# Kernel optimization log

Measured on AMD Instinct MI355X. Metric: run time of the kernel, lower is better.

## Reference

```python
import jax, jax.numpy as jnp
import numpy as np
from jax import lax

N_NODES = 19
N_FILT = 8
CONV_CH = N_NODES * N_FILT  # 152
T = 512
POOL = 4
T_POOL = T // POOL  # 128
GCN_OUT = 16
FLAT = N_NODES * GCN_OUT * T_POOL  # 38912
HID = 128
N_CLS = 2
BN_EPS = 1e-5


def setup_inputs() -> dict:
    key = jax.random.key(0)
    ks = jax.random.split(key, 12)
    B = 1024
    x = jax.random.normal(ks[0], (B, N_NODES, T), dtype=jnp.float32)
    # grouped Conv1d(19 -> 152, k=5, groups=19): kernel (out_ch, in_ch/groups=1, k)
    conv_w = jax.random.normal(ks[1], (CONV_CH, 1, 5), dtype=jnp.float32) * 0.2
    conv_b = jax.random.normal(ks[2], (CONV_CH,), dtype=jnp.float32) * 0.05
    bn_gamma = jnp.ones((CONV_CH,), jnp.float32)
    bn_beta = jnp.zeros((CONV_CH,), jnp.float32)
    bn_mean = jax.random.normal(ks[3], (CONV_CH,), dtype=jnp.float32) * 0.1
    bn_var = jax.random.uniform(ks[4], (CONV_CH,), dtype=jnp.float32, minval=0.5, maxval=1.5)
    adj = jax.random.uniform(ks[5], (N_NODES, N_NODES), dtype=jnp.float32)
    gcn_w = jax.random.normal(ks[6], (GCN_OUT, N_FILT), dtype=jnp.float32) * (1.0 / np.sqrt(N_FILT))
    gcn_b = jnp.zeros((GCN_OUT,), jnp.float32)
    w1 = jax.random.normal(ks[7], (HID, FLAT), dtype=jnp.float32) * (1.0 / np.sqrt(FLAT))
    b1 = jnp.zeros((HID,), jnp.float32)
    w2 = jax.random.normal(ks[8], (N_CLS, HID), dtype=jnp.float32) * (1.0 / np.sqrt(HID))
    b2 = jnp.zeros((N_CLS,), jnp.float32)
    return dict(x=x, conv_w=conv_w, conv_b=conv_b, bn_gamma=bn_gamma, bn_beta=bn_beta,
                bn_mean=bn_mean, bn_var=bn_var, adj=adj, gcn_w=gcn_w, gcn_b=gcn_b,
                w1=w1, b1=b1, w2=w2, b2=b2)


def reference(x, conv_w, conv_b, bn_gamma, bn_beta, bn_mean, bn_var, adj,
              gcn_w, gcn_b, w1, b1, w2, b2):
    B = x.shape[0]
    # depthwise temporal conv: [B,19,T] -> [B,152,T]
    h = lax.conv_general_dilated(x, conv_w, window_strides=(1,), padding=[(2, 2)],
                                 feature_group_count=N_NODES,
                                 dimension_numbers=('NCW', 'OIW', 'NCW'))
    h = h + conv_b[None, :, None]
    # BatchNorm1d (eval mode: running stats) + ReLU, fused elementwise
    inv = bn_gamma / jnp.sqrt(bn_var + BN_EPS)
    h = jax.nn.relu(h * inv[None, :, None] + (bn_beta - bn_mean * inv)[None, :, None])
    # MaxPool1d(4): [B,152,512] -> [B,152,128]
    h = h.reshape(B, CONV_CH, T_POOL, POOL).max(axis=-1)
    # view -> [B,19,8,128]
    h = h.reshape(B, N_NODES, N_FILT, T_POOL)
    # softmax adjacency aggregation: bift = A_ij * bjft
    A = jax.nn.softmax(adj, axis=1)
    support = jnp.einsum('ij,bjft->bift', A, h)
    # permute to [B,19,128,8], linear 8->16, ReLU
    g = jax.nn.relu(jnp.einsum('bnft,of->bnto', support, gcn_w) + gcn_b)
    # classifier: flatten -> Linear(38912,128) -> ReLU -> (Dropout eval=identity) -> Linear(128,2)
    flat = g.reshape(B, FLAT)
    hid = jax.nn.relu(flat @ w1.T + b1)
    return hid @ w2.T + b2
```

## Files before the change

### kernel.cpp

```cpp
#include <hip/hip_runtime.h>

#define NB    1024
#define NN    19
#define NF    8
#define CCH   152
#define TLEN  512
#define TP    128
#define GO    16
#define KFLAT 38912
#define HID   128
#define NCLS  2
#define NROWS (NB*TP)
#define KC    152
#define KP    160
#define NJP   20
#define NOUT  304
#define GW    320
#define KW    (TP*GW)

#define KTILE 1024
#define NKT   (KW / KTILE)

typedef float  f32x4  __attribute__((ext_vector_type(4)));
typedef __bf16 bf16x8 __attribute__((ext_vector_type(8)));
typedef __bf16 bf16x4 __attribute__((ext_vector_type(4)));
typedef unsigned short u16x8 __attribute__((ext_vector_type(8)));

__global__ __launch_bounds__(256) void prep_small(
    const float* __restrict__ adj,
    const float* __restrict__ bn_gamma, const float* __restrict__ bn_beta,
    const float* __restrict__ bn_mean,  const float* __restrict__ bn_var,
    const float* __restrict__ conv_b,
    float* __restrict__ A_g, float* __restrict__ bnS, float* __restrict__ bnB)
{
    const int tid = threadIdx.x;
    if (tid < NN) {
        float v[NN];
        float m = -1e30f;
        #pragma unroll
        for (int j = 0; j < NN; ++j) { v[j] = adj[tid * NN + j]; m = fmaxf(m, v[j]); }
        float s = 0.f;
        #pragma unroll
        for (int j = 0; j < NN; ++j) { v[j] = expf(v[j] - m); s += v[j]; }
        float rc = 1.f / s;
        #pragma unroll
        for (int j = 0; j < NN; ++j) A_g[tid * NN + j] = v[j] * rc;
    }
    if (tid >= 64 && tid < 64 + CCH) {
        int c = tid - 64;
        float inv = bn_gamma[c] * rsqrtf(bn_var[c] + 1e-5f);
        bnS[c] = inv;
        bnB[c] = conv_b[c] * inv + bn_beta[c] - bn_mean[c] * inv;
    }
}

__global__ __launch_bounds__(256) void prep_m2(
    const float* __restrict__ A_g, const float* __restrict__ gcn_w,
    __bf16* __restrict__ m2g)
{
    int i = blockIdx.x * 256 + threadIdx.x;
    if (i >= GW * KP) return;
    int c = i / KP, k = i - c * KP;
    float v = 0.f;
    if (c < NOUT && k < KC) {
        int n = c >> 4, o = c & 15;
        int j = k >> 3, f = k & 7;
        v = A_g[n * NN + j] * gcn_w[o * NF + f];
    }
    m2g[i] = (__bf16)v;
}

__global__ __launch_bounds__(640) void conv_mix(
    const float* __restrict__ x,
    const float* __restrict__ conv_w,
    const float* __restrict__ bnS, const float* __restrict__ bnB,
    const __bf16* __restrict__ m2g,
    const float* __restrict__ gcn_b,
    __bf16* __restrict__ g2)
{
    __shared__ __align__(16) __bf16 Hs[NJP][64][8];

    const int tid  = threadIdx.x;
    const int lane = tid & 63, w = tid >> 6;
    const int b    = blockIdx.x >> 1;
    const int half = blockIdx.x & 1;
    const int tp0  = half * 64;

    {
        const int T = tp0 + lane;
        #pragma unroll
        for (int k = 0; k < 2; ++k) {
            const int n = 2 * w + k;
            if (n < NN) {
                const float* xr = x + ((size_t)b * NN + n) * TLEN;
                float4 L0 = {0.f, 0.f, 0.f, 0.f};
                float4 L2 = {0.f, 0.f, 0.f, 0.f};
                if (T > 0)   L0 = *(const float4*)(xr + 4 * T - 4);
                float4 L1 =       *(const float4*)(xr + 4 * T);
                if (T < 127) L2 = *(const float4*)(xr + 4 * T + 4);
                float xv[9] = {L0.z, L0.w, L1.x, L1.y, L1.z, L1.w, L2.x, L2.y, L2.z};

                const float* cw = conv_w + n * (NF * 5);
                const float* Sp = bnS + n * NF;
                const float* Bp = bnB + n * NF;
                union { __bf16 h[8]; u16x8 v; } hv;
                #pragma unroll
                for (int f = 0; f < NF; ++f) {
                    float w0 = cw[f*5+0], w1 = cw[f*5+1], w2 = cw[f*5+2], w3 = cw[f*5+3], w4 = cw[f*5+4];
                    float s = Sp[f], bb = Bp[f];
                    float m = -1e30f;
                    #pragma unroll
                    for (int p = 0; p < 4; ++p) {
                        float a = xv[p]*w0 + xv[p+1]*w1 + xv[p+2]*w2 + xv[p+3]*w3 + xv[p+4]*w4;
                        m = fmaxf(m, a * s + bb);
                    }
                    hv.h[f] = (__bf16)fmaxf(m, 0.f);
                }
                *(u16x8*)&Hs[n][lane][0] = hv.v;
            } else {
                u16x8 z = {0,0,0,0,0,0,0,0};
                *(u16x8*)&Hs[NJP - 1][lane][0] = z;
            }
        }
    }

    const int arow = lane & 15;
    const int jg   = lane >> 4;
    const int ct0  = w * 2;
    const float4 gbv = *(const float4*)(gcn_b + jg * 4);

    bf16x8 mf[2][5];
    #pragma unroll
    for (int ct = 0; ct < 2; ++ct)
        #pragma unroll
        for (int ks = 0; ks < 5; ++ks)
            mf[ct][ks] = *(const bf16x8*)(
                m2g + (size_t)((ct0 + ct) * 16 + arow) * KP + ks * 32 + jg * 8);

    __syncthreads();

    for (int it = 0; it < 4; ++it) {
        const int tl = it * 16 + arow;

        bf16x8 af[5];
        #pragma unroll
        for (int ks = 0; ks < 5; ++ks)
            af[ks] = *(const bf16x8*)&Hs[ks * 4 + jg][tl][0];

        f32x4 acc[2];
        #pragma unroll
        for (int ct = 0; ct < 2; ++ct) acc[ct] = (f32x4){0.f, 0.f, 0.f, 0.f};

        #pragma unroll
        for (int ks = 0; ks < 5; ++ks)
            #pragma unroll
            for (int ct = 0; ct < 2; ++ct)
                acc[ct] = __builtin_amdgcn_mfma_f32_16x16x32_bf16(mf[ct][ks], af[ks], acc[ct], 0, 0, 0);

        __bf16* gp = g2 + ((size_t)b * TP + tp0 + tl) * GW + ct0 * 16 + jg * 4;
        #pragma unroll
        for (int ct = 0; ct < 2; ++ct) {
            bf16x4 v;
            v[0] = (__bf16)fmaxf(acc[ct][0] + gbv.x, 0.f);
            v[1] = (__bf16)fmaxf(acc[ct][1] + gbv.y, 0.f);
            v[2] = (__bf16)fmaxf(acc[ct][2] + gbv.z, 0.f);
            v[3] = (__bf16)fmaxf(acc[ct][3] + gbv.w, 0.f);
            *(bf16x4*)(gp + ct * 16) = v;
        }
    }
}

__global__ __launch_bounds__(256) void w1_permute(
    const float* __restrict__ w1, __bf16* __restrict__ w1p)
{
    int i = blockIdx.x * 256 + threadIdx.x;
    if (i >= HID * (KW / 8)) return;
    int j = i / 5120, rem = i - j * 5120;
    int t = rem / 40, c8 = rem - t * 40;
    bf16x8 r;
    if (c8 < 38) {
        int n = c8 >> 1, o0 = (c8 & 1) * 8;
        const float* src = w1 + (size_t)j * KFLAT + n * 2048 + t * 16 + o0;
        #pragma unroll
        for (int e = 0; e < 8; ++e) r[e] = (__bf16)src[e];
    } else {
        #pragma unroll
        for (int e = 0; e < 8; ++e) r[e] = (__bf16)0.f;
    }
    *(bf16x8*)(w1p + (size_t)i * 8) = r;
}

__global__ __launch_bounds__(256) void gemm_fc1(
    const __bf16* __restrict__ gmat,
    const __bf16* __restrict__ wmat,
    float* __restrict__ partial)
{
    __shared__ __align__(16) __bf16 At[128][40];
    __shared__ __align__(16) __bf16 Bt[128][40];

    const int tid = threadIdx.x;
    const int b0 = blockIdx.x * 128;
    const int k0 = blockIdx.y * KTILE;

    const int lane = tid & 63;
    const int w = tid >> 6;
    const int wm = (w >> 1) * 64;
    const int wn = (w & 1) * 64;

    const int srow = tid >> 2;
    const int soct = tid & 3;

    f32x4 acc[4][4];
    #pragma unroll
    for (int m = 0; m < 4; ++m)
        #pragma unroll
        for (int n = 0; n < 4; ++n) acc[m][n] = (f32x4){0.f, 0.f, 0.f, 0.f};

    const int arow = lane & 15;
    const int aoct = (lane >> 4) * 8;

    for (int ks = 0; ks < KTILE / 32; ++ks) {
        const int gk = k0 + ks * 32 + soct * 8;
        *(u16x8*)&At[srow     ][soct * 8] = *(const u16x8*)(gmat + (size_t)(b0 + srow     ) * KW + gk);
        *(u16x8*)&At[srow + 64][soct * 8] = *(const u16x8*)(gmat + (size_t)(b0 + srow + 64) * KW + gk);
        *(u16x8*)&Bt[srow     ][soct * 8] = *(const u16x8*)(wmat + (size_t)(srow     ) * KW + gk);
        *(u16x8*)&Bt[srow + 64][soct * 8] = *(const u16x8*)(wmat + (size_t)(srow + 64) * KW + gk);
        __syncthreads();

        bf16x8 af[4], bfr[4];
        #pragma unroll
        for (int m = 0; m < 4; ++m) af[m]  = *(const bf16x8*)&At[wm + m * 16 + arow][aoct];
        #pragma unroll
        for (int n = 0; n < 4; ++n) bfr[n] = *(const bf16x8*)&Bt[wn + n * 16 + arow][aoct];
        #pragma unroll
        for (int m = 0; m < 4; ++m)
            #pragma unroll
            for (int n = 0; n < 4; ++n)
                acc[m][n] = __builtin_amdgcn_mfma_f32_16x16x32_bf16(af[m], bfr[n], acc[m][n], 0, 0, 0);
        __syncthreads();
    }

    float* pout = partial + (size_t)blockIdx.y * (NB * HID);
    #pragma unroll
    for (int m = 0; m < 4; ++m) {
        const int rbase = b0 + wm + m * 16 + (lane >> 4) * 4;
        #pragma unroll
        for (int n = 0; n < 4; ++n) {
            const int col = wn + n * 16 + (lane & 15);
            #pragma unroll
            for (int r = 0; r < 4; ++r)
                pout[(size_t)(rbase + r) * HID + col] = acc[m][n][r];
        }
    }
}

__global__ __launch_bounds__(128) void reduce_fc2(
    const float* __restrict__ partial,
    const float* __restrict__ b1,
    const float* __restrict__ w2,
    const float* __restrict__ b2,
    float* __restrict__ out)
{
    __shared__ float red0[128], red1[128];
    const int b = blockIdx.x, j = threadIdx.x;
    float s = b1[j];
    #pragma unroll 4
    for (int p = 0; p < NKT; ++p) s += partial[(size_t)p * (NB * HID) + b * HID + j];
    float h = fmaxf(s, 0.f);
    red0[j] = h * w2[j];
    red1[j] = h * w2[HID + j];
    __syncthreads();
    for (int off = 64; off > 0; off >>= 1) {
        if (j < off) { red0[j] += red0[j + off]; red1[j] += red1[j + off]; }
        __syncthreads();
    }
    if (j == 0) {
        out[b * 2 + 0] = red0[0] + b2[0];
        out[b * 2 + 1] = red1[0] + b2[1];
    }
}

extern "C" void kernel_launch(void* const* d_in, const int* in_sizes, int n_in,
                              void* d_out, int out_size, void* d_ws, size_t ws_size,
                              hipStream_t stream) {
    const float* x        = (const float*)d_in[0];
    const float* conv_w   = (const float*)d_in[1];
    const float* conv_b   = (const float*)d_in[2];
    const float* bn_gamma = (const float*)d_in[3];
    const float* bn_beta  = (const float*)d_in[4];
    const float* bn_mean  = (const float*)d_in[5];
    const float* bn_var   = (const float*)d_in[6];
    const float* adj      = (const float*)d_in[7];
    const float* gcn_w    = (const float*)d_in[8];
    const float* gcn_b    = (const float*)d_in[9];
    const float* w1       = (const float*)d_in[10];
    const float* b1       = (const float*)d_in[11];
    const float* w2       = (const float*)d_in[12];
    const float* b2       = (const float*)d_in[13];
    float* out = (float*)d_out;

    char* ws = (char*)d_ws;
    __bf16* g2   = (__bf16*)ws;
    __bf16* w1p  = (__bf16*)(ws + 83886080);
    float*  part = (float*)(ws + 94371840);
    __bf16* m2g  = (__bf16*)(ws + 125829120);
    float*  A_g  = (float*)(ws + 125931520);
    float*  bnS  = (float*)(ws + 125933568);
    float*  bnB  = (float*)(ws + 125934592);

    prep_small<<<dim3(1), dim3(256), 0, stream>>>(
        adj, bn_gamma, bn_beta, bn_mean, bn_var, conv_b, A_g, bnS, bnB);
    prep_m2<<<dim3(200), dim3(256), 0, stream>>>(A_g, gcn_w, m2g);
    conv_mix<<<dim3(NB * 2), dim3(640), 0, stream>>>(x, conv_w, bnS, bnB, m2g, gcn_b, g2);
    w1_permute<<<dim3(HID * (KW / 8) / 256), dim3(256), 0, stream>>>(w1, w1p);
    gemm_fc1<<<dim3(8, NKT), dim3(256), 0, stream>>>(g2, w1p, part);
    reduce_fc2<<<dim3(NB), dim3(128), 0, stream>>>(part, b1, w2, b2, out);
}
```

Before: 117.4 us.

## Make conv_mix persistent over four tiles with double-buffered LDS and prefetch

Each conv_mix block now handles four (batch, half) tiles instead of one, with a double-buffered LDS H tile. The x loads for the next tile are issued before the MFMA mix of the current tile, and the next conv is computed into the other buffer. This amortizes the per-block m2g fragment loads and launch overhead and overlaps global loads with MFMA work. In exchange the grid shrinks by four and register pressure rises from the prefetched float4s.

```diff
diff --git a/kernel.cpp b/kernel.cpp
--- a/kernel.cpp
+++ b/kernel.cpp
@@ -17,6 +17,7 @@
 #define NOUT  304
 #define GW    320
 #define KW    (TP*GW)
+#define NTPB  4
 
 #define KTILE 1024
 #define NKT   (KW / KTILE)
@@ -78,56 +79,17 @@
     const float* __restrict__ gcn_b,
     __bf16* __restrict__ g2)
 {
-    __shared__ __align__(16) __bf16 Hs[NJP][64][8];
+    __shared__ __align__(16) __bf16 Hs[2][NJP][64][8];
 
     const int tid  = threadIdx.x;
     const int lane = tid & 63, w = tid >> 6;
-    const int b    = blockIdx.x >> 1;
-    const int half = blockIdx.x & 1;
-    const int tp0  = half * 64;
-
-    {
-        const int T = tp0 + lane;
-        #pragma unroll
-        for (int k = 0; k < 2; ++k) {
-            const int n = 2 * w + k;
-            if (n < NN) {
-                const float* xr = x + ((size_t)b * NN + n) * TLEN;
-                float4 L0 = {0.f, 0.f, 0.f, 0.f};
-                float4 L2 = {0.f, 0.f, 0.f, 0.f};
-                if (T > 0)   L0 = *(const float4*)(xr + 4 * T - 4);
-                float4 L1 =       *(const float4*)(xr + 4 * T);
-                if (T < 127) L2 = *(const float4*)(xr + 4 * T + 4);
-                float xv[9] = {L0.z, L0.w, L1.x, L1.y, L1.z, L1.w, L2.x, L2.y, L2.z};
-
-                const float* cw = conv_w + n * (NF * 5);
-                const float* Sp = bnS + n * NF;
-                const float* Bp = bnB + n * NF;
-                union { __bf16 h[8]; u16x8 v; } hv;
-                #pragma unroll
-                for (int f = 0; f < NF; ++f) {
-                    float w0 = cw[f*5+0], w1 = cw[f*5+1], w2 = cw[f*5+2], w3 = cw[f*5+3], w4 = cw[f*5+4];
-                    float s = Sp[f], bb = Bp[f];
-                    float m = -1e30f;
-                    #pragma unroll
-                    for (int p = 0; p < 4; ++p) {
-                        float a = xv[p]*w0 + xv[p+1]*w1 + xv[p+2]*w2 + xv[p+3]*w3 + xv[p+4]*w4;
-                        m = fmaxf(m, a * s + bb);
-                    }
-                    hv.h[f] = (__bf16)fmaxf(m, 0.f);
-                }
-                *(u16x8*)&Hs[n][lane][0] = hv.v;
-            } else {
-                u16x8 z = {0,0,0,0,0,0,0,0};
-                *(u16x8*)&Hs[NJP - 1][lane][0] = z;
-            }
-        }
-    }
-
     const int arow = lane & 15;
     const int jg   = lane >> 4;
     const int ct0  = w * 2;
     const float4 gbv = *(const float4*)(gcn_b + jg * 4);
+    const int n0 = 2 * w, n1 = 2 * w + 1;
+
+    const int t0 = blockIdx.x * NTPB;
 
     bf16x8 mf[2][5];
     #pragma unroll
@@ -137,35 +99,94 @@
             mf[ct][ks] = *(const bf16x8*)(
                 m2g + (size_t)((ct0 + ct) * 16 + arow) * KP + ks * 32 + jg * 8);
 
+    float4 nx[3];
+    const float4 f4z = {0.f, 0.f, 0.f, 0.f};
+
+    auto LOADX = [&](int tau) {
+        const int b = tau >> 1;
+        const int T = (tau & 1) * 64 + lane;
+        const float* xr = x + ((size_t)b * NN + n0) * TLEN;
+        nx[0] = (T > 0)   ? *(const float4*)(xr + 4 * T - 4) : f4z;
+        nx[1] =             *(const float4*)(xr + 4 * T);
+        nx[2] = (T < 127) ? *(const float4*)(xr + 4 * T + 4) : f4z;
+    };
+
+    auto CONV1 = [&](int buf, int n, const float4& L0, const float4& L1, const float4& L2) {
+        float xv[9] = {L0.z, L0.w, L1.x, L1.y, L1.z, L1.w, L2.x, L2.y, L2.z};
+        const float* cw = conv_w + n * (NF * 5);
+        const float* Sp = bnS + n * NF;
+        const float* Bp = bnB + n * NF;
+        union { __bf16 h[8]; u16x8 v; } hv;
+        #pragma unroll
+        for (int f = 0; f < NF; ++f) {
+            float w0 = cw[f*5+0], w1 = cw[f*5+1], w2 = cw[f*5+2], w3 = cw[f*5+3], w4 = cw[f*5+4];
+            float s = Sp[f], bb = Bp[f];
+            float m = -1e30f;
+            #pragma unroll
+            for (int p = 0; p < 4; ++p) {
+                float a = xv[p]*w0 + xv[p+1]*w1 + xv[p+2]*w2 + xv[p+3]*w3 + xv[p+4]*w4;
+                m = fmaxf(m, a * s + bb);
+            }
+            hv.h[f] = (__bf16)fmaxf(m, 0.f);
+        }
+        *(u16x8*)&Hs[buf][n][lane][0] = hv.v;
+    };
+
+    auto CONV = [&](int buf, int tau) {
+        const int b = tau >> 1;
+        const int T = (tau & 1) * 64 + lane;
+        CONV1(buf, n0, nx[0], nx[1], nx[2]);
+        if (n1 < NN) {
+            const float* xr = x + ((size_t)b * NN + n1) * TLEN;
+            float4 L0 = (T > 0)   ? *(const float4*)(xr + 4 * T - 4) : f4z;
+            float4 L1 =             *(const float4*)(xr + 4 * T);
+            float4 L2 = (T < 127) ? *(const float4*)(xr + 4 * T + 4) : f4z;
+            CONV1(buf, n1, L0, L1, L2);
+        } else {
+            u16x8 z = {0,0,0,0,0,0,0,0};
+            *(u16x8*)&Hs[buf][NJP - 1][lane][0] = z;
+        }
+    };
+
+    auto MIX = [&](int buf, int tau) {
+        const int b = tau >> 1, tp0 = (tau & 1) * 64;
+        for (int it = 0; it < 4; ++it) {
+            const int tl = it * 16 + arow;
+            bf16x8 af[5];
+            #pragma unroll
+            for (int ks = 0; ks < 5; ++ks)
+                af[ks] = *(const bf16x8*)&Hs[buf][ks * 4 + jg][tl][0];
+            f32x4 acc[2];
+            #pragma unroll
+            for (int ct = 0; ct < 2; ++ct) acc[ct] = (f32x4){0.f, 0.f, 0.f, 0.f};
+            #pragma unroll
+            for (int ks = 0; ks < 5; ++ks)
+                #pragma unroll
+                for (int ct = 0; ct < 2; ++ct)
+                    acc[ct] = __builtin_amdgcn_mfma_f32_16x16x32_bf16(mf[ct][ks], af[ks], acc[ct], 0, 0, 0);
+            __bf16* gp = g2 + ((size_t)b * TP + tp0 + tl) * GW + ct0 * 16 + jg * 4;
+            #pragma unroll
+            for (int ct = 0; ct < 2; ++ct) {
+                bf16x4 v;
+                v[0] = (__bf16)fmaxf(acc[ct][0] + gbv.x, 0.f);
+                v[1] = (__bf16)fmaxf(acc[ct][1] + gbv.y, 0.f);
+                v[2] = (__bf16)fmaxf(acc[ct][2] + gbv.z, 0.f);
+                v[3] = (__bf16)fmaxf(acc[ct][3] + gbv.w, 0.f);
+                *(bf16x4*)(gp + ct * 16) = v;
+            }
+        }
+    };
+
+    LOADX(t0);
+    CONV(0, t0);
     __syncthreads();
 
-    for (int it = 0; it < 4; ++it) {
-        const int tl = it * 16 + arow;
-
-        bf16x8 af[5];
-        #pragma unroll
-        for (int ks = 0; ks < 5; ++ks)
-            af[ks] = *(const bf16x8*)&Hs[ks * 4 + jg][tl][0];
-
-        f32x4 acc[2];
-        #pragma unroll
-        for (int ct = 0; ct < 2; ++ct) acc[ct] = (f32x4){0.f, 0.f, 0.f, 0.f};
-
-        #pragma unroll
-        for (int ks = 0; ks < 5; ++ks)
-            #pragma unroll
-            for (int ct = 0; ct < 2; ++ct)
-                acc[ct] = __builtin_amdgcn_mfma_f32_16x16x32_bf16(mf[ct][ks], af[ks], acc[ct], 0, 0, 0);
-
-        __bf16* gp = g2 + ((size_t)b * TP + tp0 + tl) * GW + ct0 * 16 + jg * 4;
-        #pragma unroll
-        for (int ct = 0; ct < 2; ++ct) {
-            bf16x4 v;
-            v[0] = (__bf16)fmaxf(acc[ct][0] + gbv.x, 0.f);
-            v[1] = (__bf16)fmaxf(acc[ct][1] + gbv.y, 0.f);
-            v[2] = (__bf16)fmaxf(acc[ct][2] + gbv.z, 0.f);
-            v[3] = (__bf16)fmaxf(acc[ct][3] + gbv.w, 0.f);
-            *(bf16x4*)(gp + ct * 16) = v;
+    for (int i = 0; i < NTPB; ++i) {
+        if (i + 1 < NTPB) LOADX(t0 + i + 1);
+        MIX(i & 1, t0 + i);
+        if (i + 1 < NTPB) {
+            CONV((i + 1) & 1, t0 + i + 1);
+            __syncthreads();
         }
     }
 }
@@ -311,7 +332,7 @@
     prep_small<<<dim3(1), dim3(256), 0, stream>>>(
         adj, bn_gamma, bn_beta, bn_mean, bn_var, conv_b, A_g, bnS, bnB);
     prep_m2<<<dim3(200), dim3(256), 0, stream>>>(A_g, gcn_w, m2g);
-    conv_mix<<<dim3(NB * 2), dim3(640), 0, stream>>>(x, conv_w, bnS, bnB, m2g, gcn_b, g2);
+    conv_mix<<<dim3(NB * 2 / NTPB), dim3(640), 0, stream>>>(x, conv_w, bnS, bnB, m2g, gcn_b, g2);
     w1_permute<<<dim3(HID * (KW / 8) / 256), dim3(256), 0, stream>>>(w1, w1p);
     gemm_fc1<<<dim3(8, NKT), dim3(256), 0, stream>>>(g2, w1p, part);
     reduce_fc2<<<dim3(NB), dim3(128), 0, stream>>>(part, b1, w2, b2, out);
```

After: 115.6 us. About the same (-1.6%).
